# Performance work log

Measured on AMD Instinct MI355X. Metric: run time of the kernel, lower is better.

The kernel has to match this reference:

```python
import jax, jax.numpy as jnp
import numpy as np

B, S, D, H = 8, 2048, 256, 4
HD = D // H  # 64
EPS = 1e-5


def setup_inputs() -> dict:
    key = jax.random.key(0)
    ks = jax.random.split(key, 16)
    sc = 0.05
    return {
        "descriptors": jax.random.normal(ks[0], (B, S, D), jnp.float32),
        "source": jax.random.normal(ks[1], (B, S, D), jnp.float32),
        "mask": jnp.ones((B, S), jnp.int32),
        # attention projections (stored as [in, out])
        "q_w": jax.random.normal(ks[2], (D, D), jnp.float32) * sc,
        "q_b": jnp.zeros((D,), jnp.float32),
        "k_w": jax.random.normal(ks[3], (D, D), jnp.float32) * sc,
        "k_b": jnp.zeros((D,), jnp.float32),
        "v_w": jax.random.normal(ks[4], (D, D), jnp.float32) * sc,
        "v_b": jnp.zeros((D,), jnp.float32),
        "o_w": jax.random.normal(ks[5], (D, D), jnp.float32) * sc,
        "o_b": jnp.zeros((D,), jnp.float32),
        # MLP layer 0: 2D -> 2D, BatchNorm1d (eval mode) + ReLU
        "m0_w": jax.random.normal(ks[6], (2 * D, 2 * D), jnp.float32) * sc,
        "m0_b": jnp.zeros((2 * D,), jnp.float32),
        "bn_g": jax.random.uniform(ks[7], (2 * D,), jnp.float32, 0.5, 1.5),
        "bn_b": jax.random.normal(ks[8], (2 * D,), jnp.float32) * 0.1,
        "bn_m": jax.random.normal(ks[9], (2 * D,), jnp.float32) * 0.1,
        "bn_v": jax.random.uniform(ks[10], (2 * D,), jnp.float32, 0.5, 1.5),
        # MLP layer 1: 2D -> D, no activation
        "m1_w": jax.random.normal(ks[11], (2 * D, D), jnp.float32) * sc,
        "m1_b": jnp.zeros((D,), jnp.float32),
    }


def reference(descriptors, source, mask, q_w, q_b, k_w, k_b, v_w, v_b, o_w, o_b,
              m0_w, m0_b, bn_g, bn_b, bn_m, bn_v, m1_w, m1_b):
    # Multi-head cross-attention: query=descriptors, key=value=source
    q = (descriptors @ q_w + q_b).reshape(B, S, H, HD).transpose(0, 2, 1, 3)  # [B,H,S,HD]
    k = (source @ k_w + k_b).reshape(B, S, H, HD).transpose(0, 2, 1, 3)
    v = (source @ v_w + v_b).reshape(B, S, H, HD).transpose(0, 2, 1, 3)

    scores = jnp.einsum("bhqd,bhkd->bhqk", q, k) / jnp.sqrt(jnp.float32(HD))
    scores = jnp.where(mask[:, None, None, :] == 0, -1e9, scores)
    probs = jax.nn.softmax(scores.astype(jnp.float32), axis=-1)  # [B,H,S,S]

    ctx = jnp.einsum("bhqk,bhkd->bhqd", probs, v)  # [B,H,S,HD]
    ctx = ctx.transpose(0, 2, 1, 3).reshape(B, S, D)
    attn_out = ctx @ o_w + o_b  # out_proj

    # concat + MLP (Linear -> BatchNorm1d(eval) -> ReLU -> Linear)
    h = jnp.concatenate([descriptors, attn_out], axis=-1)  # [B,S,2D]
    h = h @ m0_w + m0_b
    h = (h - bn_m) * jax.lax.rsqrt(bn_v + EPS) * bn_g + bn_b  # per-channel BN
    h = jax.nn.relu(h)
    h = h @ m1_w + m1_b  # [B,S,D]
    return h
```

## Files before the change

### kernel.cpp

```cpp
#include <hip/hip_runtime.h>

#define NB 8
#define NS 2048
#define ND 256
#define NH 4
#define NHD 64
#define ND2 512
#define NM (NB * NS)
#define PITCH 72
#define C1 0.18033688f

typedef __attribute__((ext_vector_type(8))) short          bf16x8;
typedef __attribute__((ext_vector_type(4))) float          f32x4;
typedef unsigned short ushort_t;
typedef unsigned int   uint_t;

#define MFMA16(a, b, c) __builtin_amdgcn_mfma_f32_16x16x32_bf16(a, b, c, 0, 0, 0)

#if __has_builtin(__builtin_amdgcn_exp2f)
#define EXP2(x) __builtin_amdgcn_exp2f(x)
#else
#define EXP2(x) exp2f(x)
#endif

static __device__ inline uint_t pack2bf(float a, float b) {
    union { float f; uint_t u; } x, y; x.f = a; y.f = b;
    return __builtin_amdgcn_perm(y.u + 0x8000u, x.u + 0x8000u, 0x07060302u);
}
static __device__ inline ushort_t f2bf(float f) {
    union { float f; uint_t u; } x; x.f = f;
    return (ushort_t)((x.u + 0x7FFFu + ((x.u >> 16) & 1u)) >> 16);
}


static __device__ inline void femit(ushort_t* buf, int n, int k, float v) {
    const int kc = k >> 5;
    const int lane = (((k >> 3) & 3) << 4) | (n & 15);
    const int j = k & 7;
    buf[((size_t)(((n >> 4) * 16 + kc) * 64 + lane)) * 8 + j] = f2bf(v);
}

__global__ __launch_bounds__(256) void prep(
    const float* __restrict__ desc, const float* __restrict__ srcp,
    const int* __restrict__ mask,
    const float* __restrict__ q_w, const float* __restrict__ k_w,
    const float* __restrict__ v_w, const float* __restrict__ m1_w,
    const float* __restrict__ o_w, const float* __restrict__ o_b,
    const float* __restrict__ m0_w, const float* __restrict__ m0_b,
    const float* __restrict__ bng, const float* __restrict__ bnb,
    const float* __restrict__ bnm, const float* __restrict__ bnv,
    ushort_t* __restrict__ descF, ushort_t* __restrict__ srcF,
    ushort_t* __restrict__ qwF, ushort_t* __restrict__ kwF,
    ushort_t* __restrict__ vwF, ushort_t* __restrict__ m1F,
    ushort_t* __restrict__ m0fF, float* __restrict__ biasf,
    float* __restrict__ mbias)
{
    __shared__ float ow[256];
    const int blk = blockIdx.x;
    const int t = threadIdx.x;

    if (blk < 4096) {
        const int y = blk >> 11, x = blk & 2047;
        const float* src = y ? srcp : desc;
        ushort_t* dst    = y ? srcF : descF;
        const int g = x * 256 + t;
        const int lane = g & 63, ci = g >> 6;
        const int kc = ci & 7, r16 = ci >> 3;
        const int row = r16 * 16 + (lane & 15);
        const int c0  = kc * 32 + (lane >> 4) * 8;
        const float* p = src + (size_t)row * ND + c0;
        float4 a = *(const float4*)p;
        float4 b = *(const float4*)(p + 4);
        uint4 pk;
        pk.x = pack2bf(a.x, a.y); pk.y = pack2bf(a.z, a.w);
        pk.z = pack2bf(b.x, b.y); pk.w = pack2bf(b.z, b.w);
        *(uint4*)(dst + (size_t)g * 8) = pk;
    } else if (blk < 4352) {
        const int wb = blk - 4096;
        const int y = wb >> 6, x = wb & 63;
        const float* src; ushort_t* dst; int K, N; float sc = 1.0f;
        switch (y) {
            case 0: src = q_w; dst = qwF; K = 256; N = 256; sc = C1; break;
            case 1: src = k_w; dst = kwF; K = 256; N = 256; break;
            case 2: src = v_w; dst = vwF; K = 256; N = 256; break;
            default: src = m1_w; dst = m1F; K = 512; N = 256; break;
        }
        const int g = x * 256 + t;
        if (g >= (N * K) / 8) return;
        const int lane = g & 63, ci = g >> 6;
        const int lgck = (K == 512) ? 4 : 3;
        const int kc = ci & ((1 << lgck) - 1), n16 = ci >> lgck;
        const int n  = n16 * 16 + (lane & 15);
        const int k0 = kc * 32 + (lane >> 4) * 8;
        float f[8];
#pragma unroll
        for (int j = 0; j < 8; j++) f[j] = src[(size_t)(k0 + j) * N + n] * sc;
        uint4 pk;
        pk.x = pack2bf(f[0], f[1]); pk.y = pack2bf(f[2], f[3]);
        pk.z = pack2bf(f[4], f[5]); pk.w = pack2bf(f[6], f[7]);
        *(uint4*)(dst + (size_t)g * 8) = pk;
    } else if (blk < 4416) {
        const int i = (blk - 4352) * 256 + t;
        mbias[i] = mask[i] ? 0.0f : -1e9f;
    } else if (blk < 4672) {
        const int i = blk - 4416;
        ow[t] = o_w[i * 256 + t];
        __syncthreads();
        float f0 = 0.f, f1 = 0.f;
#pragma unroll 4
        for (int j = 0; j < 256; j++) {
            const float w = ow[j];
            f0 += w * m0_w[(size_t)(256 + j) * 512 + t];
            f1 += w * m0_w[(size_t)(256 + j) * 512 + t + 256];
        }
        const float A0v = bng[t] * rsqrtf(bnv[t] + 1e-5f);
        const float A1v = bng[t + 256] * rsqrtf(bnv[t + 256] + 1e-5f);
        femit(m0fF, t, 256 + i, f0 * A0v);
        femit(m0fF, t + 256, 256 + i, f1 * A1v);
        femit(m0fF, t, i, m0_w[(size_t)i * 512 + t] * A0v);
        femit(m0fF, t + 256, i, m0_w[(size_t)i * 512 + t + 256] * A1v);
    } else {
        const int bb = blk - 4672;
        const int n  = bb * 32 + (t >> 3);
        const int jp = t & 7;
        float s = 0.f;
#pragma unroll 4
        for (int j = jp * 32; j < jp * 32 + 32; j++)
            s += o_b[j] * m0_w[(size_t)(256 + j) * 512 + n];
        s += __shfl_xor(s, 1);
        s += __shfl_xor(s, 2);
        s += __shfl_xor(s, 4);
        if (jp == 0) {
            const float A = bng[n] * rsqrtf(bnv[n] + 1e-5f);
            biasf[n] = (m0_b[n] + s - bnm[n]) * A + bnb[n];
        }
    }
}

template <int KC, int AK, bool NAT, int MT>
static __device__ inline void core(
    const ushort_t* __restrict__ A0, const ushort_t* __restrict__ A1,
    const ushort_t* __restrict__ WF, int t16, int n16, f32x4 acc[MT][4])
{
    const int lane = threadIdx.x & 63;
#pragma unroll
    for (int kc = 0; kc < KC; kc++) {
        const ushort_t* Ab = (kc < AK) ? A0 : A1;
        const int kca = (kc < AK) ? kc : kc - AK;
        bf16x8 af[MT], wf[4];
#pragma unroll
        for (int mt = 0; mt < MT; mt++)
            af[mt] = *(const bf16x8*)(Ab + ((size_t)((t16 + mt) * AK + kca) * 64 + lane) * 8);
#pragma unroll
        for (int nt = 0; nt < 4; nt++)
            wf[nt] = *(const bf16x8*)(WF + ((size_t)((n16 + nt) * KC + kc) * 64 + lane) * 8);
#pragma unroll
        for (int mt = 0; mt < MT; mt++)
#pragma unroll
            for (int nt = 0; nt < 4; nt++) {
                if (NAT) acc[mt][nt] = MFMA16(af[mt], wf[nt], acc[mt][nt]);
                else     acc[mt][nt] = MFMA16(wf[nt], af[mt], acc[mt][nt]);
            }
    }
}

__global__ __launch_bounds__(256) void qkv_frag(
    const ushort_t* __restrict__ descF, const ushort_t* __restrict__ srcF,
    const ushort_t* __restrict__ qwF, const ushort_t* __restrict__ kwF,
    const ushort_t* __restrict__ vwF,
    const float* __restrict__ q_b, const float* __restrict__ k_b,
    const float* __restrict__ v_b,
    ushort_t* __restrict__ qF, ushort_t* __restrict__ kF,
    ushort_t* __restrict__ vF)
{
    const int t = threadIdx.x, w = t >> 6;
    const int lq = t & 15, lg = (t & 63) >> 4;
    const int h    = blockIdx.x;
    const int tok0 = (blockIdx.y << 8) + (w << 6);
    const int t16  = tok0 >> 4, n16 = h << 2;
    const int z    = blockIdx.z;

    f32x4 acc[4][4];
#pragma unroll
    for (int mt = 0; mt < 4; mt++)
#pragma unroll
        for (int nt = 0; nt < 4; nt++) acc[mt][nt] = (f32x4){0.f, 0.f, 0.f, 0.f};

    if (z == 2) {
        core<8, 8, true, 4>(srcF, srcF, vwF, t16, n16, acc);
#pragma unroll
        for (int nt = 0; nt < 4; nt++) {
            const int dvh = nt * 16 + lq;
            const float bs = v_b[h * 64 + dvh];
#pragma unroll
            for (int mt = 0; mt < 4; mt++) {
                const int tok = tok0 + mt * 16 + lg * 4;
                const int b = tok >> 11, s0 = tok & 2047;
                const int bh = b * NH + h;
                uint2 pv;
                pv.x = pack2bf(acc[mt][nt][0] + bs, acc[mt][nt][1] + bs);
                pv.y = pack2bf(acc[mt][nt][2] + bs, acc[mt][nt][3] + bs);
                const size_t e = (size_t)bh * 131072 +
                    ((size_t)((dvh >> 4) * 64 + (s0 >> 5)) * 64 +
                     (((s0 >> 3) & 3) * 16 + (dvh & 15))) * 8 + (s0 & 7);
                *(uint2*)(vF + e) = pv;
            }
        }
    } else {
        const ushort_t* A = z ? srcF : descF;
        const ushort_t* W = z ? kwF : qwF;
        const float* bias = z ? k_b : q_b;
        ushort_t* dst     = z ? kF : qF;
        const float bsc   = z ? 1.0f : C1;
        core<8, 8, false, 4>(A, A, W, t16, n16, acc);
#pragma unroll
        for (int nt = 0; nt < 4; nt++) {
            const int d0 = nt * 16 + lg * 4;
            f32x4 b4 = *(const f32x4*)(bias + h * 64 + d0);
#pragma unroll
            for (int mt = 0; mt < 4; mt++) {
                const int tok = tok0 + mt * 16 + lq;
                const int b = tok >> 11, s = tok & 2047;
                const int bh = b * NH + h;
                uint2 pv;
                pv.x = pack2bf(acc[mt][nt][0] + b4[0] * bsc,
                               acc[mt][nt][1] + b4[1] * bsc);
                pv.y = pack2bf(acc[mt][nt][2] + b4[2] * bsc,
                               acc[mt][nt][3] + b4[3] * bsc);
                const size_t e = (size_t)bh * 131072 +
                    ((size_t)((s >> 4) * 2 + (d0 >> 5)) * 64 +
                     (((d0 >> 3) & 3) * 16 + lq)) * 8 + (d0 & 7);
                *(uint2*)(dst + e) = pv;
            }
        }
    }
}

__global__ __launch_bounds__(256) void mlp0_frag(
    const ushort_t* __restrict__ descF, const ushort_t* __restrict__ ctxF,
    const ushort_t* __restrict__ m0fF, const float* __restrict__ biasf,
    ushort_t* __restrict__ hF)
{
    const int t = threadIdx.x, w = t >> 6;
    const int lq = t & 15, lg = (t & 63) >> 4;
    const int n0   = blockIdx.x << 6;
    const int tok0 = (blockIdx.y << 8) + (w << 6);
    const int t16  = tok0 >> 4, n16 = n0 >> 4;

    f32x4 acc[4][4];
#pragma unroll
    for (int mt = 0; mt < 4; mt++)
#pragma unroll
        for (int nt = 0; nt < 4; nt++) acc[mt][nt] = (f32x4){0.f, 0.f, 0.f, 0.f};

    core<16, 8, false, 4>(descF, ctxF, m0fF, t16, n16, acc);

#pragma unroll
    for (int nt = 0; nt < 4; nt++) {
        const int c0 = n0 + nt * 16 + lg * 4;
        f32x4 b4 = *(const f32x4*)(biasf + c0);
#pragma unroll
        for (int mt = 0; mt < 4; mt++) {
            const int tok = tok0 + mt * 16 + lq;
            uint2 pv;
            pv.x = pack2bf(fmaxf(acc[mt][nt][0] + b4[0], 0.f),
                           fmaxf(acc[mt][nt][1] + b4[1], 0.f));
            pv.y = pack2bf(fmaxf(acc[mt][nt][2] + b4[2], 0.f),
                           fmaxf(acc[mt][nt][3] + b4[3], 0.f));
            const size_t e = ((size_t)((tok >> 4) * 16 + (c0 >> 5)) * 64 +
                              (((c0 >> 3) & 3) * 16 + lq)) * 8 + (c0 & 7);
            *(uint2*)(hF + e) = pv;
        }
    }
}

__global__ __launch_bounds__(256) void mlp1_frag(
    const ushort_t* __restrict__ hF, const ushort_t* __restrict__ m1F,
    const float* __restrict__ m1_b, float* __restrict__ out)
{
    const int t = threadIdx.x, w = t >> 6;
    const int lq = t & 15, lg = (t & 63) >> 4;
    const int n0   = blockIdx.x << 6;
    const int tok0 = (blockIdx.y << 7) + (w << 5);
    const int t16  = tok0 >> 4, n16 = n0 >> 4;

    f32x4 acc[2][4];
#pragma unroll
    for (int mt = 0; mt < 2; mt++)
#pragma unroll
        for (int nt = 0; nt < 4; nt++) acc[mt][nt] = (f32x4){0.f, 0.f, 0.f, 0.f};

    core<16, 16, false, 2>(hF, hF, m1F, t16, n16, acc);

#pragma unroll
    for (int nt = 0; nt < 4; nt++) {
        const int c0 = n0 + nt * 16 + lg * 4;
        f32x4 b4 = *(const f32x4*)(m1_b + c0);
#pragma unroll
        for (int mt = 0; mt < 2; mt++) {
            const int tok = tok0 + mt * 16 + lq;
            f32x4 o4;
#pragma unroll
            for (int j = 0; j < 4; j++) o4[j] = acc[mt][nt][j] + b4[j];
            *(f32x4*)(out + (size_t)tok * ND + c0) = o4;
        }
    }
}

__global__ __launch_bounds__(256) void attn_frag(
    const ushort_t* __restrict__ qF, const ushort_t* __restrict__ kF,
    const ushort_t* __restrict__ vF, const float* __restrict__ mbias,
    ushort_t* __restrict__ ctxF)
{
    __shared__ ushort_t Pl[8][16 * PITCH];

    const int t = threadIdx.x, w = t >> 6, lane = t & 63;
    const int lq = t & 15, lg = lane >> 4;
    const int flat = blockIdx.x + (blockIdx.y << 4) + (blockIdx.z << 6);
    const int bh = (flat & 7) + (((flat >> 7) & 3) << 3);
    const int qb = (flat >> 3) & 15;
    const int b = bh >> 2, h = bh & 3;
    (void)b; (void)h;

    const ushort_t* qh = qF + (size_t)bh * 131072;
    const ushort_t* kh = kF + (size_t)bh * 131072;
    const ushort_t* vh = vF + (size_t)bh * 131072;
    const float* mrow = mbias + (bh >> 2) * NS;
    const int qrow0 = qb * 128 + w * 32;
    const int q16 = qrow0 >> 4;

    bf16x8 qf[2][2];
#pragma unroll
    for (int qt = 0; qt < 2; qt++)
#pragma unroll
        for (int kc = 0; kc < 2; kc++)
            qf[qt][kc] = *(const bf16x8*)(qh + ((size_t)((q16 + qt) * 2 + kc) * 64 + lane) * 8);

    f32x4 o[2][4];
#pragma unroll
    for (int qt = 0; qt < 2; qt++)
#pragma unroll
        for (int dt = 0; dt < 4; dt++) o[qt][dt] = (f32x4){0.f, 0.f, 0.f, 0.f};
    float l_part[2] = {0.0f, 0.0f};

    bf16x8 ka[4][2];
#pragma unroll
    for (int kt = 0; kt < 4; kt++)
#pragma unroll
        for (int kk = 0; kk < 2; kk++)
            ka[kt][kk] = *(const bf16x8*)(kh + ((size_t)((kt * 2 + kk) * 64 + lane)) * 8);

    for (int key0 = 0; key0 < NS; key0 += 64) {
        bf16x8 vf[4][2];
        const ushort_t* vb = vh + (size_t)(key0 >> 5) * 512;
#pragma unroll
        for (int dt = 0; dt < 4; dt++)
#pragma unroll
            for (int kh2 = 0; kh2 < 2; kh2++)
                vf[dt][kh2] = *(const bf16x8*)(vb +
                    ((size_t)((dt * 64 + kh2) * 64 + lane)) * 8);
        f32x4 mb[4];
#pragma unroll
        for (int kt = 0; kt < 4; kt++)
            mb[kt] = *(const f32x4*)(mrow + key0 + kt * 16 + lg * 4);

        f32x4 st[2][4];
#pragma unroll
        for (int qt = 0; qt < 2; qt++)
#pragma unroll
            for (int kt = 0; kt < 4; kt++) {
                f32x4 a = (f32x4){0.f, 0.f, 0.f, 0.f};
                a = MFMA16(ka[kt][0], qf[qt][0], a);
                a = MFMA16(ka[kt][1], qf[qt][1], a);
                st[qt][kt] = a;
            }

        const int keyn = (key0 + 64) & (NS - 1);
        const ushort_t* kb = kh + (size_t)keyn * 64;
        bf16x8 kn[4][2];
#pragma unroll
        for (int kt = 0; kt < 4; kt++)
#pragma unroll
            for (int kk = 0; kk < 2; kk++)
                kn[kt][kk] = *(const bf16x8*)(kb + ((size_t)((kt * 2 + kk) * 64 + lane)) * 8);

#pragma unroll
        for (int qt = 0; qt < 2; qt++) {
            float ls = 0.0f;
#pragma unroll
            for (int kt = 0; kt < 4; kt++) {
                float pr[4];
#pragma unroll
                for (int r = 0; r < 4; r++) {
                    const float p = EXP2(st[qt][kt][r] + mb[kt][r]);
                    ls += p;
                    pr[r] = p;
                }
                uint2 pv;
                pv.x = pack2bf(pr[0], pr[1]);
                pv.y = pack2bf(pr[2], pr[3]);
                *(uint2*)&Pl[w * 2 + qt][lq * PITCH + kt * 16 + lg * 4] = pv;
            }
            l_part[qt] += ls;
        }

        bf16x8 pf[2][2];
#pragma unroll
        for (int qt = 0; qt < 2; qt++)
#pragma unroll
            for (int kh2 = 0; kh2 < 2; kh2++)
                pf[qt][kh2] = *(const bf16x8*)&Pl[w * 2 + qt][lq * PITCH + kh2 * 32 + lg * 8];

#pragma unroll
        for (int dt = 0; dt < 4; dt++)
#pragma unroll
            for (int kh2 = 0; kh2 < 2; kh2++)
#pragma unroll
                for (int qt = 0; qt < 2; qt++)
                    o[qt][dt] = MFMA16(vf[dt][kh2], pf[qt][kh2], o[qt][dt]);

#pragma unroll
        for (int kt = 0; kt < 4; kt++)
#pragma unroll
            for (int kk = 0; kk < 2; kk++)
                ka[kt][kk] = kn[kt][kk];
    }

#pragma unroll
    for (int qt = 0; qt < 2; qt++) {
        float ls = l_part[qt];
        ls += __shfl_xor(ls, 16);
        ls += __shfl_xor(ls, 32);
        const float li = 1.0f / ls;
        const int tok16 = (bh >> 2) * 128 + q16 + qt;
#pragma unroll
        for (int dt = 0; dt < 4; dt++) {
            const int c = (bh & 3) * 64 + dt * 16 + lg * 4;
            uint2 pv;
            pv.x = pack2bf(o[qt][dt][0] * li, o[qt][dt][1] * li);
            pv.y = pack2bf(o[qt][dt][2] * li, o[qt][dt][3] * li);
            const size_t e = ((size_t)(tok16 * 8 + (c >> 5)) * 64 +
                              (((c >> 3) & 3) * 16 + lq)) * 8 + (c & 7);
            *(uint2*)(ctxF + e) = pv;
        }
    }
}

extern "C" void kernel_launch(void* const* d_in, const int* in_sizes, int n_in,
                              void* d_out, int out_size, void* d_ws, size_t ws_size,
                              hipStream_t stream)
{
    (void)in_sizes; (void)n_in; (void)out_size; (void)ws_size;
    const float* desc = (const float*)d_in[0];
    const float* srcp = (const float*)d_in[1];
    const int*   mask = (const int*)d_in[2];
    const float* q_w  = (const float*)d_in[3];
    const float* q_b  = (const float*)d_in[4];
    const float* k_w  = (const float*)d_in[5];
    const float* k_b  = (const float*)d_in[6];
    const float* v_w  = (const float*)d_in[7];
    const float* v_b  = (const float*)d_in[8];
    const float* o_w  = (const float*)d_in[9];
    const float* o_b  = (const float*)d_in[10];
    const float* m0_w = (const float*)d_in[11];
    const float* m0_b = (const float*)d_in[12];
    const float* bng  = (const float*)d_in[13];
    const float* bnb  = (const float*)d_in[14];
    const float* bnm  = (const float*)d_in[15];
    const float* bnv  = (const float*)d_in[16];
    const float* m1_w = (const float*)d_in[17];
    const float* m1_b = (const float*)d_in[18];
    float* out = (float*)d_out;

    const size_t ASZ = (size_t)NM * ND;
    ushort_t* descF = (ushort_t*)d_ws;
    ushort_t* srcF  = descF + ASZ;
    ushort_t* qF    = descF + 2 * ASZ;
    ushort_t* kF    = descF + 3 * ASZ;
    ushort_t* vF    = descF + 4 * ASZ;
    ushort_t* qwF   = descF + 5 * ASZ;
    ushort_t* kwF   = qwF + 65536;
    ushort_t* vwF   = kwF + 65536;
    ushort_t* m1F   = vwF + 65536;
    ushort_t* m0fF  = m1F + 131072;
    float*    biasf = (float*)(m0fF + 262144);
    float*    mbias = biasf + 512;
    ushort_t* ctxF  = srcF;
    ushort_t* hF    = qF;

    const dim3 blk(256);

    prep<<<dim3(4688), blk, 0, stream>>>(
        desc, srcp, mask, q_w, k_w, v_w, m1_w, o_w, o_b, m0_w, m0_b,
        bng, bnb, bnm, bnv, descF, srcF, qwF, kwF, vwF, m1F, m0fF, biasf, mbias);

    qkv_frag<<<dim3(4, NM / 256, 3), blk, 0, stream>>>(
        descF, srcF, qwF, kwF, vwF, q_b, k_b, v_b, qF, kF, vF);
    attn_frag<<<dim3(NS / 128, NH, NB), blk, 0, stream>>>(qF, kF, vF, mbias, ctxF);
    mlp0_frag<<<dim3(8, NM / 256), blk, 0, stream>>>(descF, ctxF, m0fF, biasf, hF);
    mlp1_frag<<<dim3(4, NM / 128), blk, 0, stream>>>(hF, m1F, m1_b, out);
}
```

Measured before the change: 240.6 us.

## Rewrite attention inner loop with 32x32 MFMA and register-only P transpose

Switches the attention kernel from 16x16x32 to 32x32x16 bf16 MFMA tiles, with each wave handling 32 query rows as a single tile. The softmax probabilities are no longer staged through LDS. They are converted with v_cvt_pk_bf16 and rearranged across lanes with v_permlane32_swap so they can feed the PV MFMA straight from registers. The mask bias is folded into the accumulator init, and s_setprio hints are placed around the MFMA blocks. This aims to remove LDS round-trips and cut instruction overhead, but relies on gfx950-specific instructions and on correct fragment index mapping.

```diff
diff --git a/kernel.cpp b/kernel.cpp
--- a/kernel.cpp
+++ b/kernel.cpp
@@ -7,15 +7,16 @@
 #define NHD 64
 #define ND2 512
 #define NM (NB * NS)
-#define PITCH 72
 #define C1 0.18033688f
 
 typedef __attribute__((ext_vector_type(8))) short          bf16x8;
 typedef __attribute__((ext_vector_type(4))) float          f32x4;
+typedef __attribute__((ext_vector_type(16))) float         f32x16;
 typedef unsigned short ushort_t;
 typedef unsigned int   uint_t;
 
 #define MFMA16(a, b, c) __builtin_amdgcn_mfma_f32_16x16x32_bf16(a, b, c, 0, 0, 0)
+#define MFMA32(a, b, c) __builtin_amdgcn_mfma_f32_32x32x16_bf16(a, b, c, 0, 0, 0)
 
 #if __has_builtin(__builtin_amdgcn_exp2f)
 #define EXP2(x) __builtin_amdgcn_exp2f(x)
@@ -30,6 +31,14 @@
 static __device__ inline ushort_t f2bf(float f) {
     union { float f; uint_t u; } x; x.f = f;
     return (ushort_t)((x.u + 0x7FFFu + ((x.u >> 16) & 1u)) >> 16);
+}
+static __device__ inline uint_t cvtpk_bf16(float a, float b) {
+    uint_t r;
+    asm("v_cvt_pk_bf16_f32 %0, %1, %2" : "=v"(r) : "v"(a), "v"(b));
+    return r;
+}
+static __device__ inline void plswap(uint_t &a, uint_t &b) {
+    asm("v_permlane32_swap_b32 %0, %1" : "+v"(a), "+v"(b));
 }
 
 
@@ -312,138 +321,138 @@
     const ushort_t* __restrict__ vF, const float* __restrict__ mbias,
     ushort_t* __restrict__ ctxF)
 {
-    __shared__ ushort_t Pl[8][16 * PITCH];
-
     const int t = threadIdx.x, w = t >> 6, lane = t & 63;
-    const int lq = t & 15, lg = lane >> 4;
+    const int q = lane & 31, h = lane >> 5;
     const int flat = blockIdx.x + (blockIdx.y << 4) + (blockIdx.z << 6);
     const int bh = (flat & 7) + (((flat >> 7) & 3) << 3);
     const int qb = (flat >> 3) & 15;
-    const int b = bh >> 2, h = bh & 3;
-    (void)b; (void)h;
 
     const ushort_t* qh = qF + (size_t)bh * 131072;
     const ushort_t* kh = kF + (size_t)bh * 131072;
     const ushort_t* vh = vF + (size_t)bh * 131072;
     const float* mrow = mbias + (bh >> 2) * NS;
+
     const int qrow0 = qb * 128 + w * 32;
-    const int q16 = qrow0 >> 4;
-
-    bf16x8 qf[2][2];
-#pragma unroll
-    for (int qt = 0; qt < 2; qt++)
-#pragma unroll
-        for (int kc = 0; kc < 2; kc++)
-            qf[qt][kc] = *(const bf16x8*)(qh + ((size_t)((q16 + qt) * 2 + kc) * 64 + lane) * 8);
-
-    f32x4 o[2][4];
-#pragma unroll
-    for (int qt = 0; qt < 2; qt++)
-#pragma unroll
-        for (int dt = 0; dt < 4; dt++) o[qt][dt] = (f32x4){0.f, 0.f, 0.f, 0.f};
-    float l_part[2] = {0.0f, 0.0f};
-
-    bf16x8 ka[4][2];
-#pragma unroll
-    for (int kt = 0; kt < 4; kt++)
-#pragma unroll
-        for (int kk = 0; kk < 2; kk++)
-            ka[kt][kk] = *(const bf16x8*)(kh + ((size_t)((kt * 2 + kk) * 64 + lane)) * 8);
+    const int tok = qrow0 + q;
+
+    bf16x8 qf[4];
+#pragma unroll
+    for (int st = 0; st < 4; st++)
+        qf[st] = *(const bf16x8*)(qh +
+            ((size_t)(((tok >> 4) * 2 + (st >> 1)) * 64 +
+                      ((st * 2 + h) & 3) * 16 + (tok & 15))) * 8);
+
+    f32x16 o[2];
+#pragma unroll
+    for (int dt = 0; dt < 2; dt++)
+#pragma unroll
+        for (int j = 0; j < 16; j++) o[dt][j] = 0.f;
+    float l_part = 0.0f;
+
+    bf16x8 ka[2][4];
+#pragma unroll
+    for (int kt = 0; kt < 2; kt++)
+#pragma unroll
+        for (int st = 0; st < 4; st++) {
+            const int key = kt * 32 + q;
+            ka[kt][st] = *(const bf16x8*)(kh +
+                ((size_t)(((key >> 4) * 2 + (st >> 1)) * 64 +
+                          ((st * 2 + h) & 3) * 16 + (key & 15))) * 8);
+        }
 
     for (int key0 = 0; key0 < NS; key0 += 64) {
-        bf16x8 vf[4][2];
-        const ushort_t* vb = vh + (size_t)(key0 >> 5) * 512;
-#pragma unroll
-        for (int dt = 0; dt < 4; dt++)
-#pragma unroll
-            for (int kh2 = 0; kh2 < 2; kh2++)
-                vf[dt][kh2] = *(const bf16x8*)(vb +
-                    ((size_t)((dt * 64 + kh2) * 64 + lane)) * 8);
-        f32x4 mb[4];
-#pragma unroll
-        for (int kt = 0; kt < 4; kt++)
-            mb[kt] = *(const f32x4*)(mrow + key0 + kt * 16 + lg * 4);
-
-        f32x4 st[2][4];
-#pragma unroll
-        for (int qt = 0; qt < 2; qt++)
-#pragma unroll
-            for (int kt = 0; kt < 4; kt++) {
-                f32x4 a = (f32x4){0.f, 0.f, 0.f, 0.f};
-                a = MFMA16(ka[kt][0], qf[qt][0], a);
-                a = MFMA16(ka[kt][1], qf[qt][1], a);
-                st[qt][kt] = a;
+        bf16x8 vf[2][4];
+#pragma unroll
+        for (int dt = 0; dt < 2; dt++)
+#pragma unroll
+            for (int st = 0; st < 4; st++) {
+                const int d = dt * 32 + q;
+                vf[dt][st] = *(const bf16x8*)(vh +
+                    ((size_t)(((d >> 4) * 64 + (key0 >> 5) + (st >> 1)) * 64 +
+                              ((st * 2 + h) & 3) * 16 + (d & 15))) * 8);
             }
 
+        f32x16 sa[2];
+#pragma unroll
+        for (int kt = 0; kt < 2; kt++)
+#pragma unroll
+            for (int r1 = 0; r1 < 4; r1++) {
+                f32x4 m4 = *(const f32x4*)(mrow + key0 + kt * 32 + r1 * 8 + h * 4);
+#pragma unroll
+                for (int r0 = 0; r0 < 4; r0++) sa[kt][r1 * 4 + r0] = m4[r0];
+            }
+
+        __builtin_amdgcn_s_setprio(1);
+#pragma unroll
+        for (int kt = 0; kt < 2; kt++)
+#pragma unroll
+            for (int st = 0; st < 4; st++)
+                sa[kt] = MFMA32(ka[kt][st], qf[st], sa[kt]);
+        __builtin_amdgcn_s_setprio(0);
+
         const int keyn = (key0 + 64) & (NS - 1);
-        const ushort_t* kb = kh + (size_t)keyn * 64;
-        bf16x8 kn[4][2];
-#pragma unroll
-        for (int kt = 0; kt < 4; kt++)
-#pragma unroll
-            for (int kk = 0; kk < 2; kk++)
-                kn[kt][kk] = *(const bf16x8*)(kb + ((size_t)((kt * 2 + kk) * 64 + lane)) * 8);
-
-#pragma unroll
-        for (int qt = 0; qt < 2; qt++) {
-            float ls = 0.0f;
-#pragma unroll
-            for (int kt = 0; kt < 4; kt++) {
-                float pr[4];
-#pragma unroll
-                for (int r = 0; r < 4; r++) {
-                    const float p = EXP2(st[qt][kt][r] + mb[kt][r]);
-                    ls += p;
-                    pr[r] = p;
+#pragma unroll
+        for (int kt = 0; kt < 2; kt++)
+#pragma unroll
+            for (int st = 0; st < 4; st++) {
+                const int key = keyn + kt * 32 + q;
+                ka[kt][st] = *(const bf16x8*)(kh +
+                    ((size_t)(((key >> 4) * 2 + (st >> 1)) * 64 +
+                              ((st * 2 + h) & 3) * 16 + (key & 15))) * 8);
+            }
+
+        uint_t W[2][4][2];
+#pragma unroll
+        for (int kt = 0; kt < 2; kt++)
+#pragma unroll
+            for (int r1 = 0; r1 < 4; r1++)
+#pragma unroll
+                for (int wv = 0; wv < 2; wv++) {
+                    const float p0 = EXP2(sa[kt][r1 * 4 + wv * 2]);
+                    const float p1 = EXP2(sa[kt][r1 * 4 + wv * 2 + 1]);
+                    l_part += p0 + p1;
+                    W[kt][r1][wv] = cvtpk_bf16(p0, p1);
                 }
-                uint2 pv;
-                pv.x = pack2bf(pr[0], pr[1]);
-                pv.y = pack2bf(pr[2], pr[3]);
-                *(uint2*)&Pl[w * 2 + qt][lq * PITCH + kt * 16 + lg * 4] = pv;
-            }
-            l_part[qt] += ls;
-        }
-
-        bf16x8 pf[2][2];
-#pragma unroll
-        for (int qt = 0; qt < 2; qt++)
-#pragma unroll
-            for (int kh2 = 0; kh2 < 2; kh2++)
-                pf[qt][kh2] = *(const bf16x8*)&Pl[w * 2 + qt][lq * PITCH + kh2 * 32 + lg * 8];
-
-#pragma unroll
-        for (int dt = 0; dt < 4; dt++)
-#pragma unroll
-            for (int kh2 = 0; kh2 < 2; kh2++)
-#pragma unroll
-                for (int qt = 0; qt < 2; qt++)
-                    o[qt][dt] = MFMA16(vf[dt][kh2], pf[qt][kh2], o[qt][dt]);
-
-#pragma unroll
-        for (int kt = 0; kt < 4; kt++)
-#pragma unroll
-            for (int kk = 0; kk < 2; kk++)
-                ka[kt][kk] = kn[kt][kk];
+#pragma unroll
+        for (int kt = 0; kt < 2; kt++)
+#pragma unroll
+            for (int s1 = 0; s1 < 2; s1++)
+#pragma unroll
+                for (int wv = 0; wv < 2; wv++)
+                    plswap(W[kt][2 * s1][wv], W[kt][2 * s1 + 1][wv]);
+
+        __builtin_amdgcn_s_setprio(1);
+#pragma unroll
+        for (int st = 0; st < 4; st++) {
+            const int kt = st >> 1, s1 = st & 1;
+            union { uint_t u[4]; bf16x8 v; } pb;
+            pb.u[0] = W[kt][2 * s1][0];
+            pb.u[1] = W[kt][2 * s1][1];
+            pb.u[2] = W[kt][2 * s1 + 1][0];
+            pb.u[3] = W[kt][2 * s1 + 1][1];
+#pragma unroll
+            for (int dt = 0; dt < 2; dt++)
+                o[dt] = MFMA32(vf[dt][st], pb.v, o[dt]);
+        }
+        __builtin_amdgcn_s_setprio(0);
     }
 
-#pragma unroll
-    for (int qt = 0; qt < 2; qt++) {
-        float ls = l_part[qt];
-        ls += __shfl_xor(ls, 16);
-        ls += __shfl_xor(ls, 32);
-        const float li = 1.0f / ls;
-        const int tok16 = (bh >> 2) * 128 + q16 + qt;
-#pragma unroll
-        for (int dt = 0; dt < 4; dt++) {
-            const int c = (bh & 3) * 64 + dt * 16 + lg * 4;
+    l_part += __shfl_xor(l_part, 32);
+    const float li = 1.0f / l_part;
+
+    const int tok16 = (bh >> 2) * 128 + (tok >> 4);
+#pragma unroll
+    for (int dt = 0; dt < 2; dt++)
+#pragma unroll
+        for (int r1 = 0; r1 < 4; r1++) {
+            const int c = (bh & 3) * 64 + dt * 32 + r1 * 8 + h * 4;
             uint2 pv;
-            pv.x = pack2bf(o[qt][dt][0] * li, o[qt][dt][1] * li);
-            pv.y = pack2bf(o[qt][dt][2] * li, o[qt][dt][3] * li);
+            pv.x = cvtpk_bf16(o[dt][r1 * 4 + 0] * li, o[dt][r1 * 4 + 1] * li);
+            pv.y = cvtpk_bf16(o[dt][r1 * 4 + 2] * li, o[dt][r1 * 4 + 3] * li);
             const size_t e = ((size_t)(tok16 * 8 + (c >> 5)) * 64 +
-                              (((c >> 3) & 3) * 16 + lq)) * 8 + (c & 7);
+                              (((c >> 3) & 3) * 16 + (tok & 15))) * 8 + (c & 7);
             *(uint2*)(ctxF + e) = pv;
         }
-    }
 }
 
 extern "C" void kernel_launch(void* const* d_in, const int* in_sizes, int n_in,
```

Result: no change. 243.5 us (+1.2%).
